# Kernel tuning notes

Measured on AMD Instinct MI355X. Metric: run time of the kernel, lower is better.

The kernel has to match this reference:

```python
import jax, jax.numpy as jnp
import numpy as np

B, M, KD, VD = 512, 2048, 64, 64
MAX_IT = M - 1  # iteration[0].max().item() in the torch module; made static here


def setup_inputs() -> dict:
    key = jax.random.key(0)
    ks = jax.random.split(key, 8)
    new_key = jax.random.normal(ks[0], (B, KD), dtype=jnp.float32)
    new_value = jax.random.normal(ks[1], (B, VD), dtype=jnp.float32)
    key_memory = jax.random.normal(ks[2], (B, M, KD), dtype=jnp.float32)
    value_memory = jax.random.normal(ks[3], (B, M, VD), dtype=jnp.float32)
    gate = jax.random.normal(ks[4], (B, KD + 1), dtype=jnp.float32)
    iteration = jax.random.randint(ks[5], (B, 1), 1, MAX_IT + 1).astype(jnp.int64 if jax.config.jax_enable_x64 else jnp.int32)
    iteration = iteration.at[0, 0].set(MAX_IT)  # guarantee max == MAX_IT (faithful to .max().item())
    conf_w = jax.random.normal(ks[6], (1, 1), dtype=jnp.float32) * 0.1  # FCNM 1->1 linear weight
    conf_b = jnp.zeros((1,), dtype=jnp.float32)                          # FCNM 1->1 linear bias
    return {
        "new_key": new_key, "new_value": new_value,
        "key_memory": key_memory, "value_memory": value_memory,
        "gate": gate, "conf_w": conf_w, "conf_b": conf_b,
        "iteration": iteration, "max_it": MAX_IT,
    }


def reference(new_key, new_value, key_memory, value_memory, gate, conf_w, conf_b, iteration, max_it):
    b, m, kd = key_memory.shape
    vd = value_memory.shape[-1]
    it = iteration[:, 0]  # [B]

    # --- masked similarity read (vectorized form of the masked_select/scatter_ path) ---
    # memory_mask[b, n] = (n <= iteration[b])
    memory_mask = (jnp.arange(m)[None, :] <= it[:, None]).astype(key_memory.dtype)[..., None]  # [B,M,1]
    not_first = it > 1  # rows where the read actually happens; others stay zero

    vm = value_memory * memory_mask                              # [B,M,VD]
    sim = jnp.einsum('bnd,bd->bn', vm, new_value)                # [B,M]
    wv = jax.nn.softmax(sim, axis=-1)[..., None]                 # [B,M,1]
    conf = jax.nn.sigmoid(sim[..., None] * conf_w[0, 0] + conf_b[0])  # [B,M,1] (1->1 linear + sigmoid)
    km_plus_conf = jnp.concatenate([key_memory, conf], axis=-1)  # [B,M,KD+1]
    read = jnp.sum(wv * km_plus_conf, axis=1)                    # [B,KD+1]
    read = jax.nn.sigmoid(gate) * read
    new_read_key_plus_conf = jnp.where(not_first[:, None], read, jnp.zeros((), dtype=read.dtype))

    # --- resize memory to max_it + 1 slots and scatter-write the new key/value ---
    zeros_k = jnp.zeros((b, 1, kd), dtype=key_memory.dtype)
    zeros_v = jnp.zeros((b, 1, vd), dtype=value_memory.dtype)
    new_key_memory = jnp.concatenate([key_memory[:, :max_it], zeros_k], axis=1)    # [B,max_it+1,KD]
    new_value_memory = jnp.concatenate([value_memory[:, :max_it], zeros_v], axis=1)
    bidx = jnp.arange(b)
    new_key_memory = new_key_memory.at[bidx, it].set(new_key)
    new_value_memory = new_value_memory.at[bidx, it].set(new_value)

    return new_key_memory, new_value_memory, new_read_key_plus_conf
```

## Files before the change

### kernel.cpp

```cpp
#include <hip/hip_runtime.h>
#include <math.h>

#define KD 64
#define VD 64

typedef float vfloat4 __attribute__((ext_vector_type(4)));

__device__ __forceinline__ vfloat4 ntload4(const float* p) {
    return __builtin_nontemporal_load(reinterpret_cast<const vfloat4*>(p));
}
__device__ __forceinline__ void ntstore4(float* p, vfloat4 v) {
    __builtin_nontemporal_store(v, reinterpret_cast<vfloat4*>(p));
}

__global__ __launch_bounds__(256) void k1_p_valcopy(
    const float* __restrict__ value_memory,
    const float* __restrict__ new_value,
    const int*   __restrict__ iteration,
    const float* __restrict__ conf_w,
    const float* __restrict__ conf_b,
    float* __restrict__ new_value_memory,
    float* __restrict__ p_out,
    float* __restrict__ Spart,
    float* __restrict__ PCpart,
    int M, int rows_per_block, int max_it)
{
    const int blocks_per_batch = M / rows_per_block;
    const int b     = blockIdx.x / blocks_per_batch;
    const int split = blockIdx.x % blocks_per_batch;
    const int row0  = split * rows_per_block;
    const int it    = iteration[b];
    const float cw  = conf_w[0], cb = conf_b[0];

    const int tid = threadIdx.x;
    const int l   = tid & 63;
    const int w   = tid >> 6;
    const int c4  = (l & 15) * 4;
    const int rsub = w * 4 + (l >> 4);

    const vfloat4 nv = *reinterpret_cast<const vfloat4*>(new_value + (size_t)b * VD + c4);
    const float* vmb  = value_memory     + (size_t)b * M * VD;
    float*       ovmb = new_value_memory + (size_t)b * M * VD;

    float sloc = 0.f, pcloc = 0.f;
    for (int r = rsub; r < rows_per_block; r += 16) {
        const int n = row0 + r;
        vfloat4 v = ntload4(vmb + (size_t)n * VD + c4);
        float part = fmaf(v.x, nv.x, fmaf(v.y, nv.y, fmaf(v.z, nv.z, v.w * nv.w)));
        part += __shfl_xor(part, 1);
        part += __shfl_xor(part, 2);
        part += __shfl_xor(part, 4);
        part += __shfl_xor(part, 8);
        if ((l & 15) == 0) {
            const float s = (n <= it) ? part : 0.0f;
            const float p = expf(s);
            p_out[(size_t)b * M + n] = p;
            sloc  += p;
            pcloc += p * (1.0f / (1.0f + expf(-(s * cw + cb))));
        }
        vfloat4 ov;
        if (n == it)          ov = nv;
        else if (n == max_it) ov = (vfloat4){0.f, 0.f, 0.f, 0.f};
        else                  ov = v;
        ntstore4(ovmb + (size_t)n * VD + c4, ov);
    }

    __shared__ float sS[16], sPC[16];
    if ((l & 15) == 0) { sS[rsub] = sloc; sPC[rsub] = pcloc; }
    __syncthreads();
    if (tid == 0) {
        float S = 0.f, PC = 0.f;
        for (int i = 0; i < 16; ++i) { S += sS[i]; PC += sPC[i]; }
        Spart [b * blocks_per_batch + split] = S;
        PCpart[b * blocks_per_batch + split] = PC;
    }
}

__global__ __launch_bounds__(256) void k2_read_keycopy(
    const float* __restrict__ key_memory,
    const float* __restrict__ new_key,
    const float* __restrict__ p_in,
    const int*   __restrict__ iteration,
    float* __restrict__ new_key_memory,
    float* __restrict__ pread,
    int M, int rows_per_block, int max_it)
{
    const int blocks_per_batch = M / rows_per_block;
    const int b     = blockIdx.x / blocks_per_batch;
    const int split = blockIdx.x % blocks_per_batch;
    const int row0  = split * rows_per_block;
    const int it    = iteration[b];

    const int tid = threadIdx.x;
    const int l   = tid & 63;
    const int w   = tid >> 6;
    const int c4  = (l & 15) * 4;
    const int rsub = w * 4 + (l >> 4);

    const vfloat4 nk = *reinterpret_cast<const vfloat4*>(new_key + (size_t)b * KD + c4);
    const float* kmb  = key_memory     + (size_t)b * M * KD;
    float*       okmb = new_key_memory + (size_t)b * M * KD;
    const float* pb   = p_in + (size_t)b * M;

    vfloat4 acc = (vfloat4){0.f, 0.f, 0.f, 0.f};
    for (int r = rsub; r < rows_per_block; r += 16) {
        const int n = row0 + r;
        vfloat4 v = ntload4(kmb + (size_t)n * KD + c4);
        const float p = pb[n];
        acc.x = fmaf(p, v.x, acc.x); acc.y = fmaf(p, v.y, acc.y);
        acc.z = fmaf(p, v.z, acc.z); acc.w = fmaf(p, v.w, acc.w);

        vfloat4 ov;
        if (n == it)          ov = nk;
        else if (n == max_it) ov = (vfloat4){0.f, 0.f, 0.f, 0.f};
        else                  ov = v;
        ntstore4(okmb + (size_t)n * KD + c4, ov);
    }
    acc.x += __shfl_xor(acc.x, 16); acc.y += __shfl_xor(acc.y, 16);
    acc.z += __shfl_xor(acc.z, 16); acc.w += __shfl_xor(acc.w, 16);
    acc.x += __shfl_xor(acc.x, 32); acc.y += __shfl_xor(acc.y, 32);
    acc.z += __shfl_xor(acc.z, 32); acc.w += __shfl_xor(acc.w, 32);

    __shared__ float racc[4][64];
    if (l < 16) {
        racc[w][c4 + 0] = acc.x; racc[w][c4 + 1] = acc.y;
        racc[w][c4 + 2] = acc.z; racc[w][c4 + 3] = acc.w;
    }
    __syncthreads();
    if (tid < 64) {
        const float sumk = racc[0][tid] + racc[1][tid] + racc[2][tid] + racc[3][tid];
        pread[((size_t)b * blocks_per_batch + split) * 64 + tid] = sumk;
    }
}

__global__ __launch_bounds__(256) void k3_finalize(
    const float* __restrict__ pread,
    const float* __restrict__ Spart,
    const float* __restrict__ PCpart,
    const float* __restrict__ gate,
    const int*   __restrict__ iteration,
    float* __restrict__ out_read,
    int B, int splits1, int splits2)
{
    const int idx = blockIdx.x * 256 + threadIdx.x;
    if (idx >= B * (KD + 1)) return;
    const int b = idx / (KD + 1);
    const int k = idx % (KD + 1);

    float S = 0.f;
    for (int s = 0; s < splits1; ++s) S += Spart[b * splits1 + s];

    float r;
    if (k < KD) {
        r = 0.f;
        for (int s = 0; s < splits2; ++s)
            r += pread[((size_t)b * splits2 + s) * 64 + k];
    } else {
        r = 0.f;
        for (int s = 0; s < splits1; ++s) r += PCpart[b * splits1 + s];
    }
    const float g = gate[(size_t)b * (KD + 1) + k];
    float val = (1.0f / (1.0f + expf(-g))) * (r / S);
    if (iteration[b] <= 1) val = 0.0f;
    out_read[idx] = val;
}

extern "C" void kernel_launch(void* const* d_in, const int* in_sizes, int n_in,
                              void* d_out, int out_size, void* d_ws, size_t ws_size,
                              hipStream_t stream) {
    const float* new_key      = (const float*)d_in[0];
    const float* new_value    = (const float*)d_in[1];
    const float* key_memory   = (const float*)d_in[2];
    const float* value_memory = (const float*)d_in[3];
    const float* gate         = (const float*)d_in[4];
    const float* conf_w       = (const float*)d_in[5];
    const float* conf_b       = (const float*)d_in[6];
    const int*   iteration    = (const int*)d_in[7];

    const int B = in_sizes[0] / KD;
    const int M = in_sizes[2] / in_sizes[0];
    const int max_it = M - 1;

    float* out_km   = (float*)d_out;
    float* out_vm   = out_km + (size_t)B * M * KD;
    float* out_read = out_vm + (size_t)B * M * VD;

    const int RPB1 = 128;
    const int RPB2 = 256;
    const int splits1 = M / RPB1;
    const int splits2 = M / RPB2;

    float* p      = (float*)d_ws;
    float* Spart  = p + (size_t)B * M;
    float* PCpart = Spart + (size_t)B * splits1;
    float* pread  = PCpart + (size_t)B * splits1;

    k1_p_valcopy<<<B * splits1, 256, 0, stream>>>(
        value_memory, new_value, iteration, conf_w, conf_b,
        out_vm, p, Spart, PCpart, M, RPB1, max_it);

    k2_read_keycopy<<<B * splits2, 256, 0, stream>>>(
        key_memory, new_key, p, iteration, out_km, pread, M, RPB2, max_it);

    const int total = B * (KD + 1);
    k3_finalize<<<(total + 255) / 256, 256, 0, stream>>>(
        pread, Spart, PCpart, gate, iteration, out_read, B, splits1, splits2);
}
```

Measured before the change: 201.6 us.

## Fuse value similarity pass and key read pass into one streaming kernel

Merges the value-memory softmax-weight kernel and the key-memory weighted-read kernel into one kernel that streams both memories per row block. The per-row weights no longer go through a global scratch buffer, and one launch is removed. The row loop is fully unrolled over a fixed 256-row block, which raises register pressure but keeps more loads in flight.

```diff
diff --git a/kernel.cpp b/kernel.cpp
--- a/kernel.cpp
+++ b/kernel.cpp
@@ -3,6 +3,8 @@
 
 #define KD 64
 #define VD 64
+#define RPB 256
+#define RPL 16
 
 typedef float vfloat4 __attribute__((ext_vector_type(4)));
 
@@ -13,22 +15,25 @@
     __builtin_nontemporal_store(v, reinterpret_cast<vfloat4*>(p));
 }
 
-__global__ __launch_bounds__(256) void k1_p_valcopy(
+__global__ __launch_bounds__(256) void fused_stream(
     const float* __restrict__ value_memory,
+    const float* __restrict__ key_memory,
     const float* __restrict__ new_value,
+    const float* __restrict__ new_key,
     const int*   __restrict__ iteration,
     const float* __restrict__ conf_w,
     const float* __restrict__ conf_b,
     float* __restrict__ new_value_memory,
-    float* __restrict__ p_out,
+    float* __restrict__ new_key_memory,
     float* __restrict__ Spart,
     float* __restrict__ PCpart,
-    int M, int rows_per_block, int max_it)
+    float* __restrict__ pread,
+    int M, int max_it)
 {
-    const int blocks_per_batch = M / rows_per_block;
+    const int blocks_per_batch = M / RPB;
     const int b     = blockIdx.x / blocks_per_batch;
     const int split = blockIdx.x % blocks_per_batch;
-    const int row0  = split * rows_per_block;
+    const int row0  = split * RPB;
     const int it    = iteration[b];
     const float cw  = conf_w[0], cb = conf_b[0];
 
@@ -39,94 +44,65 @@
     const int rsub = w * 4 + (l >> 4);
 
     const vfloat4 nv = *reinterpret_cast<const vfloat4*>(new_value + (size_t)b * VD + c4);
+    const vfloat4 nk = *reinterpret_cast<const vfloat4*>(new_key   + (size_t)b * KD + c4);
     const float* vmb  = value_memory     + (size_t)b * M * VD;
+    const float* kmb  = key_memory       + (size_t)b * M * KD;
     float*       ovmb = new_value_memory + (size_t)b * M * VD;
+    float*       okmb = new_key_memory   + (size_t)b * M * KD;
 
     float sloc = 0.f, pcloc = 0.f;
-    for (int r = rsub; r < rows_per_block; r += 16) {
-        const int n = row0 + r;
-        vfloat4 v = ntload4(vmb + (size_t)n * VD + c4);
+    vfloat4 acc = (vfloat4){0.f, 0.f, 0.f, 0.f};
+
+    #pragma unroll
+    for (int i = 0; i < RPL; ++i) {
+        const int n = row0 + rsub + i * 16;
+        const size_t off = (size_t)n * 64 + c4;
+
+        vfloat4 v = ntload4(vmb + off);
+        vfloat4 k = ntload4(kmb + off);
+
         float part = fmaf(v.x, nv.x, fmaf(v.y, nv.y, fmaf(v.z, nv.z, v.w * nv.w)));
         part += __shfl_xor(part, 1);
         part += __shfl_xor(part, 2);
         part += __shfl_xor(part, 4);
         part += __shfl_xor(part, 8);
-        if ((l & 15) == 0) {
-            const float s = (n <= it) ? part : 0.0f;
-            const float p = expf(s);
-            p_out[(size_t)b * M + n] = p;
-            sloc  += p;
-            pcloc += p * (1.0f / (1.0f + expf(-(s * cw + cb))));
-        }
-        vfloat4 ov;
-        if (n == it)          ov = nv;
-        else if (n == max_it) ov = (vfloat4){0.f, 0.f, 0.f, 0.f};
-        else                  ov = v;
-        ntstore4(ovmb + (size_t)n * VD + c4, ov);
+
+        const float s = (n <= it) ? part : 0.0f;
+        const float p = expf(s);
+        sloc  += p;
+        pcloc += p * (1.0f / (1.0f + expf(-(s * cw + cb))));
+
+        acc.x = fmaf(p, k.x, acc.x); acc.y = fmaf(p, k.y, acc.y);
+        acc.z = fmaf(p, k.z, acc.z); acc.w = fmaf(p, k.w, acc.w);
+
+        vfloat4 ovv, ovk;
+        if (n == it)          { ovv = nv; ovk = nk; }
+        else if (n == max_it) { ovv = (vfloat4){0,0,0,0}; ovk = (vfloat4){0,0,0,0}; }
+        else                  { ovv = v;  ovk = k; }
+        ntstore4(ovmb + off, ovv);
+        ntstore4(okmb + off, ovk);
     }
 
-    __shared__ float sS[16], sPC[16];
-    if ((l & 15) == 0) { sS[rsub] = sloc; sPC[rsub] = pcloc; }
-    __syncthreads();
-    if (tid == 0) {
-        float S = 0.f, PC = 0.f;
-        for (int i = 0; i < 16; ++i) { S += sS[i]; PC += sPC[i]; }
-        Spart [b * blocks_per_batch + split] = S;
-        PCpart[b * blocks_per_batch + split] = PC;
-    }
-}
+    sloc  += __shfl_xor(sloc, 16);  sloc  += __shfl_xor(sloc, 32);
+    pcloc += __shfl_xor(pcloc, 16); pcloc += __shfl_xor(pcloc, 32);
 
-__global__ __launch_bounds__(256) void k2_read_keycopy(
-    const float* __restrict__ key_memory,
-    const float* __restrict__ new_key,
-    const float* __restrict__ p_in,
-    const int*   __restrict__ iteration,
-    float* __restrict__ new_key_memory,
-    float* __restrict__ pread,
-    int M, int rows_per_block, int max_it)
-{
-    const int blocks_per_batch = M / rows_per_block;
-    const int b     = blockIdx.x / blocks_per_batch;
-    const int split = blockIdx.x % blocks_per_batch;
-    const int row0  = split * rows_per_block;
-    const int it    = iteration[b];
-
-    const int tid = threadIdx.x;
-    const int l   = tid & 63;
-    const int w   = tid >> 6;
-    const int c4  = (l & 15) * 4;
-    const int rsub = w * 4 + (l >> 4);
-
-    const vfloat4 nk = *reinterpret_cast<const vfloat4*>(new_key + (size_t)b * KD + c4);
-    const float* kmb  = key_memory     + (size_t)b * M * KD;
-    float*       okmb = new_key_memory + (size_t)b * M * KD;
-    const float* pb   = p_in + (size_t)b * M;
-
-    vfloat4 acc = (vfloat4){0.f, 0.f, 0.f, 0.f};
-    for (int r = rsub; r < rows_per_block; r += 16) {
-        const int n = row0 + r;
-        vfloat4 v = ntload4(kmb + (size_t)n * KD + c4);
-        const float p = pb[n];
-        acc.x = fmaf(p, v.x, acc.x); acc.y = fmaf(p, v.y, acc.y);
-        acc.z = fmaf(p, v.z, acc.z); acc.w = fmaf(p, v.w, acc.w);
-
-        vfloat4 ov;
-        if (n == it)          ov = nk;
-        else if (n == max_it) ov = (vfloat4){0.f, 0.f, 0.f, 0.f};
-        else                  ov = v;
-        ntstore4(okmb + (size_t)n * KD + c4, ov);
-    }
     acc.x += __shfl_xor(acc.x, 16); acc.y += __shfl_xor(acc.y, 16);
     acc.z += __shfl_xor(acc.z, 16); acc.w += __shfl_xor(acc.w, 16);
     acc.x += __shfl_xor(acc.x, 32); acc.y += __shfl_xor(acc.y, 32);
     acc.z += __shfl_xor(acc.z, 32); acc.w += __shfl_xor(acc.w, 32);
 
+    __shared__ float sS[4], sPC[4];
     __shared__ float racc[4][64];
+    if (l == 0) { sS[w] = sloc; sPC[w] = pcloc; }
     if (l < 16) {
         racc[w][c4 + 0] = acc.x; racc[w][c4 + 1] = acc.y;
         racc[w][c4 + 2] = acc.z; racc[w][c4 + 3] = acc.w;
     }
     __syncthreads();
+    if (tid == 0) {
+        Spart [b * blocks_per_batch + split] = sS[0] + sS[1] + sS[2] + sS[3];
+        PCpart[b * blocks_per_batch + split] = sPC[0] + sPC[1] + sPC[2] + sPC[3];
+    }
     if (tid < 64) {
         const float sumk = racc[0][tid] + racc[1][tid] + racc[2][tid] + racc[3][tid];
         pread[((size_t)b * blocks_per_batch + split) * 64 + tid] = sumk;
@@ -140,7 +116,7 @@
     const float* __restrict__ gate,
     const int*   __restrict__ iteration,
     float* __restrict__ out_read,
-    int B, int splits1, int splits2)
+    int B, int splits)
 {
     const int idx = blockIdx.x * 256 + threadIdx.x;
     if (idx >= B * (KD + 1)) return;
@@ -148,16 +124,14 @@
     const int k = idx % (KD + 1);
 
     float S = 0.f;
-    for (int s = 0; s < splits1; ++s) S += Spart[b * splits1 + s];
+    for (int s = 0; s < splits; ++s) S += Spart[b * splits + s];
 
-    float r;
+    float r = 0.f;
     if (k < KD) {
-        r = 0.f;
-        for (int s = 0; s < splits2; ++s)
-            r += pread[((size_t)b * splits2 + s) * 64 + k];
+        for (int s = 0; s < splits; ++s)
+            r += pread[((size_t)b * splits + s) * 64 + k];
     } else {
-        r = 0.f;
-        for (int s = 0; s < splits1; ++s) r += PCpart[b * splits1 + s];
+        for (int s = 0; s < splits; ++s) r += PCpart[b * splits + s];
     }
     const float g = gate[(size_t)b * (KD + 1) + k];
     float val = (1.0f / (1.0f + expf(-g))) * (r / S);
@@ -180,29 +154,21 @@
     const int B = in_sizes[0] / KD;
     const int M = in_sizes[2] / in_sizes[0];
     const int max_it = M - 1;
+    const int splits = M / RPB;
 
     float* out_km   = (float*)d_out;
     float* out_vm   = out_km + (size_t)B * M * KD;
     float* out_read = out_vm + (size_t)B * M * VD;
 
-    const int RPB1 = 128;
-    const int RPB2 = 256;
-    const int splits1 = M / RPB1;
-    const int splits2 = M / RPB2;
+    float* Spart  = (float*)d_ws;
+    float* PCpart = Spart + (size_t)B * splits;
+    float* pread  = PCpart + (size_t)B * splits;
 
-    float* p      = (float*)d_ws;
-    float* Spart  = p + (size_t)B * M;
-    float* PCpart = Spart + (size_t)B * splits1;
-    float* pread  = PCpart + (size_t)B * splits1;
-
-    k1_p_valcopy<<<B * splits1, 256, 0, stream>>>(
-        value_memory, new_value, iteration, conf_w, conf_b,
-        out_vm, p, Spart, PCpart, M, RPB1, max_it);
-
-    k2_read_keycopy<<<B * splits2, 256, 0, stream>>>(
-        key_memory, new_key, p, iteration, out_km, pread, M, RPB2, max_it);
+    fused_stream<<<B * splits, 256, 0, stream>>>(
+        value_memory, key_memory, new_value, new_key, iteration,
+        conf_w, conf_b, out_vm, out_km, Spart, PCpart, pread, M, max_it);
 
     const int total = B * (KD + 1);
     k3_finalize<<<(total + 255) / 256, 256, 0, stream>>>(
-        pread, Spart, PCpart, gate, iteration, out_read, B, splits1, splits2);
+        pread, Spart, PCpart, gate, iteration, out_read, B, splits);
 }
```

Result: no change. 204.4 us (+1.3%).
